# Performance work log

Hardware: AMD Instinct MI355X
Metric: run time of the kernel (lower is better)

Reference implementation:

```python
import jax, jax.numpy as jnp
import numpy as np

B, S, D, H = 4, 2048, 1024, 16
DK = D // H


def setup_inputs() -> dict:
    key = jax.random.key(0)
    ks = jax.random.split(key, 12)
    s = 1.0 / np.sqrt(D)
    return {
        "query": jax.random.normal(ks[0], (B, S, D), jnp.float32),
        "key": jax.random.normal(ks[1], (B, S, D), jnp.float32),
        "value": jax.random.normal(ks[2], (B, S, D), jnp.float32),
        "mask": jax.random.randint(ks[3], (B, S), 0, 2, jnp.int32),
        "wq": jax.random.normal(ks[4], (D, D), jnp.float32) * s,
        "bq": jnp.zeros((D,), jnp.float32),
        "wk": jax.random.normal(ks[5], (D, D), jnp.float32) * s,
        "bk": jnp.zeros((D,), jnp.float32),
        "wv": jax.random.normal(ks[6], (D, D), jnp.float32) * s,
        "bv": jnp.zeros((D,), jnp.float32),
        "wo": jax.random.normal(ks[7], (D, D), jnp.float32) * s,
        "bo": jnp.zeros((D,), jnp.float32),
    }


def reference(query, key, value, mask, wq, bq, wk, bk, wv, bv, wo, bo):
    # torch Linear: y = x @ W.T + b
    def proj(x, w, b):
        y = jnp.einsum('bsd,ed->bse', x, w) + b
        return y.reshape(B, S, H, DK).transpose(0, 2, 1, 3)  # [B,H,S,DK]

    q = proj(query, wq, bq)
    k = proj(key, wk, bk)
    v = proj(value, wv, bv)

    scores = jnp.einsum('bhqd,bhkd->bhqk', q, k) / jnp.sqrt(jnp.float32(DK))
    m = mask[:, None, None, :]  # [B,1,1,S_kv]
    scores = jnp.where(m == 0, jnp.float32(-1e9), scores)
    attn = jax.nn.softmax(scores, axis=-1)  # dropout p=0.0 (eval)
    out = jnp.einsum('bhqk,bhkd->bhqd', attn, v)
    out = out.transpose(0, 2, 1, 3).reshape(B, S, D)
    return jnp.einsum('bsd,ed->bse', out, wo) + bo
```

## Files before the change

### kernel.cpp

```cpp
#include <hip/hip_runtime.h>
#include <hip/hip_bf16.h>

typedef __bf16 bf16;
typedef bf16 bf16x4 __attribute__((ext_vector_type(4)));
typedef bf16 bf16x8 __attribute__((ext_vector_type(8)));
typedef float f32x4 __attribute__((ext_vector_type(4)));

#define MFMA16(A,B,C) __builtin_amdgcn_mfma_f32_16x16x32_bf16(A,B,C,0,0,0)

__device__ __forceinline__ void gld_lds16(const void* g, void* l) {
  __builtin_amdgcn_global_load_lds(
      (const __attribute__((address_space(1))) void*)g,
      (__attribute__((address_space(3))) void*)l, 16, 0, 0);
}

__global__ void cast_kernel(const float* __restrict__ in, bf16* __restrict__ out, int n4) {
  int i = blockIdx.x * blockDim.x + threadIdx.x;
  if (i >= n4) return;
  float4 v = ((const float4*)in)[i];
  bf16x4 o;
  o[0] = (bf16)v.x; o[1] = (bf16)v.y; o[2] = (bf16)v.z; o[3] = (bf16)v.w;
  *(bf16x4*)(out + (size_t)i * 4) = o;
}

template<int OUT_MODE>
__global__ __launch_bounds__(256) void gemm_bt_kernel(
    const bf16* __restrict__ A, const bf16* __restrict__ Bm,
    const float* __restrict__ bias, void* __restrict__ Cout,
    int M, int N, int K, float scale)
{
  __shared__ bf16 sA[2][128 * 32];
  __shared__ bf16 sB[2][128 * 32];
  const int t = threadIdx.x;
  const int lane = t & 63, w = t >> 6;
  const int wr = w >> 1, wc = w & 1;
  const int g = lane >> 4, c = lane & 15;
  const int bm = blockIdx.y, bn = blockIdx.x;

  f32x4 acc[4][4] = {};

  const int NT = K >> 5;
  const int arow = t >> 2;
  const int acol = (t & 3) * 8;
  const bf16* aBase = A + (size_t)(bm * 128) * K;
  const bf16* bBase = Bm + (size_t)(bn * 128) * K;

  auto stage = [&](int buf, int kt) {
    const int k0 = kt * 32;
#pragma unroll
    for (int i = 0; i < 2; ++i) {
      const int row = arow + i * 64;
      gld_lds16(aBase + (size_t)row * K + k0 + acol, &sA[buf][(i * 256 + t) * 8]);
      gld_lds16(bBase + (size_t)row * K + k0 + acol, &sB[buf][(i * 256 + t) * 8]);
    }
  };

  stage(0, 0);
  __syncthreads();
  int cur = 0;
  for (int kt = 0; kt < NT; ++kt) {
    if (kt + 1 < NT) stage(cur ^ 1, kt + 1);
    bf16x8 af[4], bfr[4];
#pragma unroll
    for (int m = 0; m < 4; ++m)
      af[m] = *(const bf16x8*)&sA[cur][(wr * 64 + m * 16 + c) * 32 + g * 8];
#pragma unroll
    for (int n = 0; n < 4; ++n)
      bfr[n] = *(const bf16x8*)&sB[cur][(wc * 64 + n * 16 + c) * 32 + g * 8];
#pragma unroll
    for (int m = 0; m < 4; ++m)
#pragma unroll
      for (int n = 0; n < 4; ++n)
        acc[m][n] = MFMA16(af[m], bfr[n], acc[m][n]);
    __syncthreads();
    cur ^= 1;
  }

#pragma unroll
  for (int n = 0; n < 4; ++n) {
    const int col = bn * 128 + wc * 64 + n * 16 + c;
    const float bv = bias[col];
#pragma unroll
    for (int m = 0; m < 4; ++m) {
#pragma unroll
      for (int r = 0; r < 4; ++r) {
        const int row = bm * 128 + wr * 64 + m * 16 + g * 4 + r;
        const float val = (acc[m][n][r] + bv) * scale;
        if (OUT_MODE == 0) {
          ((bf16*)Cout)[(size_t)row * N + col] = (bf16)val;
        } else if (OUT_MODE == 1) {
          const int bb = row >> 11, s = row & 2047;
          ((bf16*)Cout)[((size_t)(bb * 1024 + col)) * 2048 + s] = (bf16)val;
        } else {
          ((float*)Cout)[(size_t)row * N + col] = val;
        }
      }
    }
  }
}

__global__ __launch_bounds__(256) void attn_kernel(
    const bf16* __restrict__ Qp, const bf16* __restrict__ Kp, const bf16* __restrict__ Vt,
    const int* __restrict__ mask, bf16* __restrict__ Out)
{
  __shared__ bf16 sK[2][64 * 64];
  __shared__ bf16 sV[2][64 * 64];
  __shared__ bf16 sP[4][32 * 72];

  const int bh = blockIdx.x;
  const int b = bh >> 4, h = bh & 15;
  const int t = threadIdx.x, lane = t & 63, w = t >> 6;
  const int g = lane >> 4, c = lane & 15;
  const int q0 = blockIdx.y * 128 + w * 32;

  const char* kBase = (const char*)(Kp + (size_t)(b * 2048) * 1024 + h * 64);
  const char* vBase = (const char*)(Vt + (size_t)(bh * 64) * 2048);

  auto stageKV = [&](int buf, int kt) {
#pragma unroll
    for (int i = 0; i < 2; ++i) {
      const int idx = i * 256 + t;
      const int row = idx >> 3;
      const int cb = ((t & 7) * 16) ^ ((row & 7) << 4);
      gld_lds16(kBase + (size_t)(kt * 64 + row) * 2048 + cb, (char*)sK[buf] + idx * 16);
      gld_lds16(vBase + (size_t)row * 4096 + kt * 128 + cb, (char*)sV[buf] + idx * 16);
    }
  };

  bf16x8 qf[2][2];
#pragma unroll
  for (int m = 0; m < 2; ++m)
#pragma unroll
    for (int ks = 0; ks < 2; ++ks)
      qf[m][ks] = *(const bf16x8*)&Qp[(size_t)(b * 2048 + q0 + m * 16 + c) * 1024 + h * 64 + ks * 32 + g * 8];

  float mrun[2][4], lrun[2][4];
  f32x4 aco[2][4] = {};
#pragma unroll
  for (int m = 0; m < 2; ++m)
#pragma unroll
    for (int r = 0; r < 4; ++r) { mrun[m][r] = -1e30f; lrun[m][r] = 0.f; }

  const int* mrow = mask + b * 2048;

  stageKV(0, 0);
  __syncthreads();
  int cur = 0;
  for (int kt = 0; kt < 32; ++kt) {
    if (kt + 1 < 32) stageKV(cur ^ 1, kt + 1);

    f32x4 s[2][4] = {};
#pragma unroll
    for (int ks = 0; ks < 2; ++ks) {
      bf16x8 kf[4];
#pragma unroll
      for (int n = 0; n < 4; ++n) {
        const int row = n * 16 + c;
        const int byt = (row * 128 + ks * 64 + g * 16) ^ ((row & 7) << 4);
        kf[n] = *(const bf16x8*)((const char*)sK[cur] + byt);
      }
#pragma unroll
      for (int m = 0; m < 2; ++m)
#pragma unroll
        for (int n = 0; n < 4; ++n)
          s[m][n] = MFMA16(qf[m][ks], kf[n], s[m][n]);
    }

    float madd[4];
#pragma unroll
    for (int n = 0; n < 4; ++n)
      madd[n] = (mrow[kt * 64 + n * 16 + c] == 0) ? -1e9f : 0.0f;
#pragma unroll
    for (int m = 0; m < 2; ++m)
#pragma unroll
      for (int n = 0; n < 4; ++n)
#pragma unroll
        for (int r = 0; r < 4; ++r) s[m][n][r] += madd[n];

#pragma unroll
    for (int m = 0; m < 2; ++m) {
#pragma unroll
      for (int r = 0; r < 4; ++r) {
        float tmax = fmaxf(fmaxf(s[m][0][r], s[m][1][r]), fmaxf(s[m][2][r], s[m][3][r]));
#pragma unroll
        for (int d = 8; d >= 1; d >>= 1) tmax = fmaxf(tmax, __shfl_xor(tmax, d, 64));
        const float mnew = fmaxf(mrun[m][r], tmax);
        const float sc = __expf(mrun[m][r] - mnew);
        mrun[m][r] = mnew;
        float rs = 0.f;
#pragma unroll
        for (int n = 0; n < 4; ++n) {
          float p = __expf(s[m][n][r] - mnew);
          s[m][n][r] = p;
          rs += p;
        }
#pragma unroll
        for (int d = 8; d >= 1; d >>= 1) rs += __shfl_xor(rs, d, 64);
        lrun[m][r] = lrun[m][r] * sc + rs;
#pragma unroll
        for (int n = 0; n < 4; ++n) aco[m][n][r] *= sc;
      }
    }

    bf16* pw = sP[w];
#pragma unroll
    for (int m = 0; m < 2; ++m)
#pragma unroll
      for (int n = 0; n < 4; ++n)
#pragma unroll
        for (int r = 0; r < 4; ++r)
          pw[(m * 16 + g * 4 + r) * 72 + n * 16 + c] = (bf16)s[m][n][r];

#pragma unroll
    for (int ks = 0; ks < 2; ++ks) {
      bf16x8 pa[2], vb[4];
#pragma unroll
      for (int m = 0; m < 2; ++m)
        pa[m] = *(const bf16x8*)&pw[(m * 16 + c) * 72 + ks * 32 + g * 8];
#pragma unroll
      for (int n = 0; n < 4; ++n) {
        const int row = n * 16 + c;
        const int byt = (row * 128 + ks * 64 + g * 16) ^ ((row & 7) << 4);
        vb[n] = *(const bf16x8*)((const char*)sV[cur] + byt);
      }
#pragma unroll
      for (int m = 0; m < 2; ++m)
#pragma unroll
        for (int n = 0; n < 4; ++n)
          aco[m][n] = MFMA16(pa[m], vb[n], aco[m][n]);
    }

    __syncthreads();
    cur ^= 1;
  }

#pragma unroll
  for (int m = 0; m < 2; ++m) {
#pragma unroll
    for (int r = 0; r < 4; ++r) {
      const int q = q0 + m * 16 + g * 4 + r;
      const float inv = 1.0f / lrun[m][r];
#pragma unroll
      for (int n = 0; n < 4; ++n) {
        const int dk = n * 16 + c;
        Out[(size_t)(b * 2048 + q) * 1024 + h * 64 + dk] = (bf16)(aco[m][n][r] * inv);
      }
    }
  }
}

extern "C" void kernel_launch(void* const* d_in, const int* in_sizes, int n_in,
                              void* d_out, int out_size, void* d_ws, size_t ws_size,
                              hipStream_t stream) {
  const float* q  = (const float*)d_in[0];
  const float* k  = (const float*)d_in[1];
  const float* v  = (const float*)d_in[2];
  const int*  msk = (const int*)d_in[3];
  const float* wq = (const float*)d_in[4];
  const float* bq = (const float*)d_in[5];
  const float* wk = (const float*)d_in[6];
  const float* bk = (const float*)d_in[7];
  const float* wv = (const float*)d_in[8];
  const float* bv = (const float*)d_in[9];
  const float* wo = (const float*)d_in[10];
  const float* bo = (const float*)d_in[11];

  bf16* ws = (bf16*)d_ws;
  const size_t NEL = 8192ull * 1024ull;
  bf16* qx  = ws;
  bf16* kx  = ws + NEL;
  bf16* vx  = ws + 2 * NEL;
  bf16* wqb = ws + 3 * NEL;
  bf16* wkb = wqb + 1048576;
  bf16* wvb = wkb + 1048576;
  bf16* wob = wvb + 1048576;
  bf16* qp  = wob + 1048576;
  bf16* kp  = qp + NEL;
  bf16* vt  = kp + NEL;
  bf16* ao  = vx;

  cast_kernel<<<8192, 256, 0, stream>>>(q, qx, 2097152);
  cast_kernel<<<8192, 256, 0, stream>>>(k, kx, 2097152);
  cast_kernel<<<8192, 256, 0, stream>>>(v, vx, 2097152);
  cast_kernel<<<1024, 256, 0, stream>>>(wq, wqb, 262144);
  cast_kernel<<<1024, 256, 0, stream>>>(wk, wkb, 262144);
  cast_kernel<<<1024, 256, 0, stream>>>(wv, wvb, 262144);
  cast_kernel<<<1024, 256, 0, stream>>>(wo, wob, 262144);

  dim3 gg(8, 64);
  gemm_bt_kernel<0><<<gg, 256, 0, stream>>>(qx, wqb, bq, qp, 8192, 1024, 1024, 0.125f);
  gemm_bt_kernel<0><<<gg, 256, 0, stream>>>(kx, wkb, bk, kp, 8192, 1024, 1024, 1.0f);
  gemm_bt_kernel<1><<<gg, 256, 0, stream>>>(vx, wvb, bv, vt, 8192, 1024, 1024, 1.0f);
  attn_kernel<<<dim3(64, 16), 256, 0, stream>>>(qp, kp, vt, msk, ao);
  gemm_bt_kernel<2><<<gg, 256, 0, stream>>>(ao, wob, bo, d_out, 8192, 1024, 1024, 1.0f);
}
```

Baseline: 520.1 us.

## Restructure attention around 32x32 MFMA with per-lane query rows and exp2 softmax

The attention kernel switches from 16x16x32 to 32x32x16 bf16 MFMA and computes S transposed (K times Q), so each lane owns one query row. Row max and row sum then need only a single xor-32 shuffle instead of four-step reductions, and mask and output accesses become vectorized. log2(e) is folded into the Q projection scale so the softmax can use exp2f. The seven cast launches are merged into two, and s_setprio is raised around MFMA bursts in both the GEMM and attention loops. The risk is higher register pressure from the 16-wide accumulators and a changed LDS access pattern for the P tile.

```diff
diff --git a/kernel.cpp b/kernel.cpp
--- a/kernel.cpp
+++ b/kernel.cpp
@@ -2,11 +2,14 @@
 #include <hip/hip_bf16.h>
 
 typedef __bf16 bf16;
+typedef bf16 bf16x2 __attribute__((ext_vector_type(2)));
 typedef bf16 bf16x4 __attribute__((ext_vector_type(4)));
 typedef bf16 bf16x8 __attribute__((ext_vector_type(8)));
 typedef float f32x4 __attribute__((ext_vector_type(4)));
+typedef float f32x16 __attribute__((ext_vector_type(16)));
 
 #define MFMA16(A,B,C) __builtin_amdgcn_mfma_f32_16x16x32_bf16(A,B,C,0,0,0)
+#define MFMA32(A,B,C) __builtin_amdgcn_mfma_f32_32x32x16_bf16(A,B,C,0,0,0)
 
 __device__ __forceinline__ void gld_lds16(const void* g, void* l) {
   __builtin_amdgcn_global_load_lds(
@@ -14,13 +17,31 @@
       (__attribute__((address_space(3))) void*)l, 16, 0, 0);
 }
 
-__global__ void cast_kernel(const float* __restrict__ in, bf16* __restrict__ out, int n4) {
-  int i = blockIdx.x * blockDim.x + threadIdx.x;
-  if (i >= n4) return;
-  float4 v = ((const float4*)in)[i];
+__global__ void cast3_kernel(const float* __restrict__ s0, const float* __restrict__ s1,
+                             const float* __restrict__ s2,
+                             bf16* __restrict__ d0, bf16* __restrict__ d1, bf16* __restrict__ d2) {
+  const int which = blockIdx.x >> 13;
+  const int i = (blockIdx.x & 8191) * 256 + threadIdx.x;
+  const float* s = which == 0 ? s0 : which == 1 ? s1 : s2;
+  bf16* d = which == 0 ? d0 : which == 1 ? d1 : d2;
+  float4 v = ((const float4*)s)[i];
   bf16x4 o;
   o[0] = (bf16)v.x; o[1] = (bf16)v.y; o[2] = (bf16)v.z; o[3] = (bf16)v.w;
-  *(bf16x4*)(out + (size_t)i * 4) = o;
+  *(bf16x4*)(d + (size_t)i * 4) = o;
+}
+
+__global__ void cast4_kernel(const float* __restrict__ s0, const float* __restrict__ s1,
+                             const float* __restrict__ s2, const float* __restrict__ s3,
+                             bf16* __restrict__ d0, bf16* __restrict__ d1,
+                             bf16* __restrict__ d2, bf16* __restrict__ d3) {
+  const int which = blockIdx.x >> 10;
+  const int i = (blockIdx.x & 1023) * 256 + threadIdx.x;
+  const float* s = which == 0 ? s0 : which == 1 ? s1 : which == 2 ? s2 : s3;
+  bf16* d = which == 0 ? d0 : which == 1 ? d1 : which == 2 ? d2 : d3;
+  float4 v = ((const float4*)s)[i];
+  bf16x4 o;
+  o[0] = (bf16)v.x; o[1] = (bf16)v.y; o[2] = (bf16)v.z; o[3] = (bf16)v.w;
+  *(bf16x4*)(d + (size_t)i * 4) = o;
 }
 
 template<int OUT_MODE>
@@ -67,11 +88,13 @@
 #pragma unroll
     for (int n = 0; n < 4; ++n)
       bfr[n] = *(const bf16x8*)&sB[cur][(wc * 64 + n * 16 + c) * 32 + g * 8];
+    __builtin_amdgcn_s_setprio(1);
 #pragma unroll
     for (int m = 0; m < 4; ++m)
 #pragma unroll
       for (int n = 0; n < 4; ++n)
         acc[m][n] = MFMA16(af[m], bfr[n], acc[m][n]);
+    __builtin_amdgcn_s_setprio(0);
     __syncthreads();
     cur ^= 1;
   }
@@ -110,7 +133,7 @@
   const int bh = blockIdx.x;
   const int b = bh >> 4, h = bh & 15;
   const int t = threadIdx.x, lane = t & 63, w = t >> 6;
-  const int g = lane >> 4, c = lane & 15;
+  const int q32 = lane & 31, hi = lane >> 5;
   const int q0 = blockIdx.y * 128 + w * 32;
 
   const char* kBase = (const char*)(Kp + (size_t)(b * 2048) * 1024 + h * 64);
@@ -127,21 +150,17 @@
     }
   };
 
-  bf16x8 qf[2][2];
-#pragma unroll
-  for (int m = 0; m < 2; ++m)
-#pragma unroll
-    for (int ks = 0; ks < 2; ++ks)
-      qf[m][ks] = *(const bf16x8*)&Qp[(size_t)(b * 2048 + q0 + m * 16 + c) * 1024 + h * 64 + ks * 32 + g * 8];
-
-  float mrun[2][4], lrun[2][4];
-  f32x4 aco[2][4] = {};
-#pragma unroll
-  for (int m = 0; m < 2; ++m)
-#pragma unroll
-    for (int r = 0; r < 4; ++r) { mrun[m][r] = -1e30f; lrun[m][r] = 0.f; }
+  bf16x8 qf[4];
+  const bf16* qrow = Qp + (size_t)(b * 2048 + q0 + q32) * 1024 + h * 64;
+#pragma unroll
+  for (int ks = 0; ks < 4; ++ks)
+    qf[ks] = *(const bf16x8*)&qrow[ks * 16 + hi * 8];
+
+  float mrun = -1e30f, lrun = 0.f;
+  f32x16 aco[2] = {};
 
   const int* mrow = mask + b * 2048;
+  bf16* pr = &sP[w][q32 * 72];
 
   stageKV(0, 0);
   __syncthreads();
@@ -149,104 +168,110 @@
   for (int kt = 0; kt < 32; ++kt) {
     if (kt + 1 < 32) stageKV(cur ^ 1, kt + 1);
 
-    f32x4 s[2][4] = {};
-#pragma unroll
-    for (int ks = 0; ks < 2; ++ks) {
-      bf16x8 kf[4];
-#pragma unroll
-      for (int n = 0; n < 4; ++n) {
-        const int row = n * 16 + c;
-        const int byt = (row * 128 + ks * 64 + g * 16) ^ ((row & 7) << 4);
-        kf[n] = *(const bf16x8*)((const char*)sK[cur] + byt);
-      }
-#pragma unroll
-      for (int m = 0; m < 2; ++m)
-#pragma unroll
-        for (int n = 0; n < 4; ++n)
-          s[m][n] = MFMA16(qf[m][ks], kf[n], s[m][n]);
-    }
-
-    float madd[4];
-#pragma unroll
-    for (int n = 0; n < 4; ++n)
-      madd[n] = (mrow[kt * 64 + n * 16 + c] == 0) ? -1e9f : 0.0f;
-#pragma unroll
-    for (int m = 0; m < 2; ++m)
-#pragma unroll
-      for (int n = 0; n < 4; ++n)
-#pragma unroll
-        for (int r = 0; r < 4; ++r) s[m][n][r] += madd[n];
-
-#pragma unroll
-    for (int m = 0; m < 2; ++m) {
-#pragma unroll
-      for (int r = 0; r < 4; ++r) {
-        float tmax = fmaxf(fmaxf(s[m][0][r], s[m][1][r]), fmaxf(s[m][2][r], s[m][3][r]));
-#pragma unroll
-        for (int d = 8; d >= 1; d >>= 1) tmax = fmaxf(tmax, __shfl_xor(tmax, d, 64));
-        const float mnew = fmaxf(mrun[m][r], tmax);
-        const float sc = __expf(mrun[m][r] - mnew);
-        mrun[m][r] = mnew;
-        float rs = 0.f;
-#pragma unroll
-        for (int n = 0; n < 4; ++n) {
-          float p = __expf(s[m][n][r] - mnew);
-          s[m][n][r] = p;
-          rs += p;
-        }
-#pragma unroll
-        for (int d = 8; d >= 1; d >>= 1) rs += __shfl_xor(rs, d, 64);
-        lrun[m][r] = lrun[m][r] * sc + rs;
-#pragma unroll
-        for (int n = 0; n < 4; ++n) aco[m][n][r] *= sc;
-      }
-    }
-
-    bf16* pw = sP[w];
-#pragma unroll
-    for (int m = 0; m < 2; ++m)
-#pragma unroll
-      for (int n = 0; n < 4; ++n)
-#pragma unroll
-        for (int r = 0; r < 4; ++r)
-          pw[(m * 16 + g * 4 + r) * 72 + n * 16 + c] = (bf16)s[m][n][r];
-
-#pragma unroll
-    for (int ks = 0; ks < 2; ++ks) {
-      bf16x8 pa[2], vb[4];
-#pragma unroll
-      for (int m = 0; m < 2; ++m)
-        pa[m] = *(const bf16x8*)&pw[(m * 16 + c) * 72 + ks * 32 + g * 8];
-#pragma unroll
-      for (int n = 0; n < 4; ++n) {
-        const int row = n * 16 + c;
-        const int byt = (row * 128 + ks * 64 + g * 16) ^ ((row & 7) << 4);
-        vb[n] = *(const bf16x8*)((const char*)sV[cur] + byt);
-      }
-#pragma unroll
-      for (int m = 0; m < 2; ++m)
-#pragma unroll
-        for (int n = 0; n < 4; ++n)
-          aco[m][n] = MFMA16(pa[m], vb[n], aco[m][n]);
+    f32x16 st[2] = {};
+#pragma unroll
+    for (int ks = 0; ks < 4; ++ks) {
+      bf16x8 k0f, k1f;
+      {
+        const int row = q32;
+        const int byt = (row * 128 + ks * 32 + hi * 16) ^ ((row & 7) << 4);
+        k0f = *(const bf16x8*)((const char*)sK[cur] + byt);
+      }
+      {
+        const int row = 32 + q32;
+        const int byt = (row * 128 + ks * 32 + hi * 16) ^ ((row & 7) << 4);
+        k1f = *(const bf16x8*)((const char*)sK[cur] + byt);
+      }
+      __builtin_amdgcn_s_setprio(1);
+      st[0] = MFMA32(k0f, qf[ks], st[0]);
+      st[1] = MFMA32(k1f, qf[ks], st[1]);
+      __builtin_amdgcn_s_setprio(0);
+    }
+
+#pragma unroll
+    for (int kf = 0; kf < 2; ++kf) {
+#pragma unroll
+      for (int q4 = 0; q4 < 4; ++q4) {
+        const int4 mm = *(const int4*)&mrow[kt * 64 + kf * 32 + q4 * 8 + hi * 4];
+        const int mv[4] = {mm.x, mm.y, mm.z, mm.w};
+#pragma unroll
+        for (int r4 = 0; r4 < 4; ++r4)
+          st[kf][q4 * 4 + r4] += (mv[r4] == 0) ? -1e9f : 0.0f;
+      }
+    }
+
+    float tmax = -1e30f;
+#pragma unroll
+    for (int i = 0; i < 16; ++i)
+      tmax = fmaxf(tmax, fmaxf(st[0][i], st[1][i]));
+    tmax = fmaxf(tmax, __shfl_xor(tmax, 32, 64));
+    const float mnew = fmaxf(mrun, tmax);
+    const float sc = exp2f(mrun - mnew);
+    mrun = mnew;
+    float rs = 0.f;
+#pragma unroll
+    for (int kf = 0; kf < 2; ++kf)
+#pragma unroll
+      for (int i = 0; i < 16; ++i) {
+        const float p = exp2f(st[kf][i] - mnew);
+        st[kf][i] = p;
+        rs += p;
+      }
+    rs += __shfl_xor(rs, 32, 64);
+    lrun = lrun * sc + rs;
+    aco[0] *= sc;
+    aco[1] *= sc;
+
+#pragma unroll
+    for (int kf = 0; kf < 2; ++kf)
+#pragma unroll
+      for (int j = 0; j < 8; ++j) {
+        const int k = kf * 32 + (j >> 1) * 8 + hi * 4 + (j & 1) * 2;
+        bf16x2 pv;
+        pv[0] = (bf16)st[kf][2 * j];
+        pv[1] = (bf16)st[kf][2 * j + 1];
+        *(bf16x2*)&pr[k] = pv;
+      }
+
+    bf16x8 pa[4];
+#pragma unroll
+    for (int kk = 0; kk < 4; ++kk)
+      pa[kk] = *(const bf16x8*)&sP[w][q32 * 72 + kk * 16 + hi * 8];
+#pragma unroll
+    for (int kk = 0; kk < 4; ++kk) {
+      bf16x8 vb0, vb1;
+      {
+        const int row = q32;
+        const int byt = (row * 128 + kk * 32 + hi * 16) ^ ((row & 7) << 4);
+        vb0 = *(const bf16x8*)((const char*)sV[cur] + byt);
+      }
+      {
+        const int row = 32 + q32;
+        const int byt = (row * 128 + kk * 32 + hi * 16) ^ ((row & 7) << 4);
+        vb1 = *(const bf16x8*)((const char*)sV[cur] + byt);
+      }
+      __builtin_amdgcn_s_setprio(1);
+      aco[0] = MFMA32(vb0, pa[kk], aco[0]);
+      aco[1] = MFMA32(vb1, pa[kk], aco[1]);
+      __builtin_amdgcn_s_setprio(0);
     }
 
     __syncthreads();
     cur ^= 1;
   }
 
-#pragma unroll
-  for (int m = 0; m < 2; ++m) {
-#pragma unroll
-    for (int r = 0; r < 4; ++r) {
-      const int q = q0 + m * 16 + g * 4 + r;
-      const float inv = 1.0f / lrun[m][r];
-#pragma unroll
-      for (int n = 0; n < 4; ++n) {
-        const int dk = n * 16 + c;
-        Out[(size_t)(b * 2048 + q) * 1024 + h * 64 + dk] = (bf16)(aco[m][n][r] * inv);
-      }
-    }
-  }
+  const float inv = 1.0f / lrun;
+  bf16* orow = Out + (size_t)(b * 2048 + q0 + q32) * 1024 + h * 64;
+#pragma unroll
+  for (int dkf = 0; dkf < 2; ++dkf)
+#pragma unroll
+    for (int q4 = 0; q4 < 4; ++q4) {
+      bf16x4 o;
+#pragma unroll
+      for (int r4 = 0; r4 < 4; ++r4)
+        o[r4] = (bf16)(aco[dkf][q4 * 4 + r4] * inv);
+      *(bf16x4*)&orow[dkf * 32 + q4 * 8 + hi * 4] = o;
+    }
 }
 
 extern "C" void kernel_launch(void* const* d_in, const int* in_sizes, int n_in,
@@ -279,16 +304,12 @@
   bf16* vt  = kp + NEL;
   bf16* ao  = vx;
 
-  cast_kernel<<<8192, 256, 0, stream>>>(q, qx, 2097152);
-  cast_kernel<<<8192, 256, 0, stream>>>(k, kx, 2097152);
-  cast_kernel<<<8192, 256, 0, stream>>>(v, vx, 2097152);
-  cast_kernel<<<1024, 256, 0, stream>>>(wq, wqb, 262144);
-  cast_kernel<<<1024, 256, 0, stream>>>(wk, wkb, 262144);
-  cast_kernel<<<1024, 256, 0, stream>>>(wv, wvb, 262144);
-  cast_kernel<<<1024, 256, 0, stream>>>(wo, wob, 262144);
-
+  cast3_kernel<<<24576, 256, 0, stream>>>(q, k, v, qx, kx, vx);
+  cast4_kernel<<<4096, 256, 0, stream>>>(wq, wk, wv, wo, wqb, wkb, wvb, wob);
+
+  const float qscale = 0.125f * 1.44269504088896f;
   dim3 gg(8, 64);
-  gemm_bt_kernel<0><<<gg, 256, 0, stream>>>(qx, wqb, bq, qp, 8192, 1024, 1024, 0.125f);
+  gemm_bt_kernel<0><<<gg, 256, 0, stream>>>(qx, wqb, bq, qp, 8192, 1024, 1024, qscale);
   gemm_bt_kernel<0><<<gg, 256, 0, stream>>>(kx, wkb, bk, kp, 8192, 1024, 1024, 1.0f);
   gemm_bt_kernel<1><<<gg, 256, 0, stream>>>(vx, wvb, bv, vt, 8192, 1024, 1024, 1.0f);
   attn_kernel<<<dim3(64, 16), 256, 0, stream>>>(qp, kp, vt, msk, ao);
```

Measured after the change: 478.9 us. -7.9%, faster.
